# Kernel tuning notes

Measured on AMD Instinct MI355X. Metric: run time of the kernel, lower is better.

The kernel has to match this reference:

```python
import jax, jax.numpy as jnp
import numpy as np

B, D_IN, D_OUT, E = 8192, 1024, 1024, 16

def setup_inputs() -> dict:
    key = jax.random.key(0)
    k1, k2, k3 = jax.random.split(key, 3)
    scale_in = 1.0 / np.sqrt(D_IN)
    return {
        "x": jax.random.normal(k1, (B, D_IN), dtype=jnp.float32),
        "Wg": jax.random.normal(k2, (D_IN, E), dtype=jnp.float32) * scale_in,
        "bg": jnp.zeros((E,), dtype=jnp.float32),
        "We": jax.random.normal(k3, (E, D_IN, D_OUT), dtype=jnp.float32) * scale_in,
        "be": jnp.zeros((E, D_OUT), dtype=jnp.float32),
    }

def reference(x, Wg, bg, We, be):
    # gate: Linear + softmax over experts  -> [B, E]
    gate_probs = jax.nn.softmax(x @ Wg + bg, axis=1)
    # all experts as one batched GEMM: [B, E, D_OUT]
    expert_outputs = jnp.einsum("bi,eio->beo", x, We) + be[None, :, :]
    # gate-weighted sum over experts -> [B, D_OUT]
    return jnp.einsum("be,beo->bo", gate_probs, expert_outputs)
```

## Files before the change

### kernel.cpp

```cpp
#include <hip/hip_runtime.h>
#include <hip/hip_bf16.h>

#define NB 8192
#define DIN 1024
#define DOUT 1024
#define NE 16

#define BM 256
#define BN 256
#define BK 64
#define NT 128

typedef __attribute__((ext_vector_type(8))) short bf16x8;
typedef __attribute__((ext_vector_type(4))) short short4_t;
typedef __attribute__((ext_vector_type(4))) float f32x4;

__device__ __forceinline__ unsigned short f32_to_bf16(float f) {
  unsigned int u = __float_as_uint(f);
  u += 0x7FFFu + ((u >> 16) & 1u);
  return (unsigned short)(u >> 16);
}

__device__ __forceinline__ void gl_lds16(const void* gp, void* lp) {
  __builtin_amdgcn_global_load_lds(
      (const __attribute__((address_space(1))) void*)gp,
      (__attribute__((address_space(3))) void*)lp, 16, 0, 0);
}

#define SB __builtin_amdgcn_sched_barrier(0)

__global__ __launch_bounds__(256) void gate_cast_kernel(
    const float* __restrict__ x, const float* __restrict__ Wg,
    const float* __restrict__ bg, float* __restrict__ gout,
    unsigned short* __restrict__ xbf) {
  const int lane = threadIdx.x & 63;
  const int wid = threadIdx.x >> 6;
  const int row = blockIdx.x * 4 + wid;

  const f32x4* xr = (const f32x4*)(x + (size_t)row * DIN);
  f32x4 xv[4];
#pragma unroll
  for (int j = 0; j < 4; ++j) xv[j] = xr[j * 64 + lane];

  float acc[NE];
#pragma unroll
  for (int e = 0; e < NE; ++e) acc[e] = 0.f;

#pragma unroll
  for (int j = 0; j < 4; ++j) {
#pragma unroll
    for (int t = 0; t < 4; ++t) {
      const int i = j * 256 + lane * 4 + t;
      const f32x4* wrow = (const f32x4*)(Wg + (size_t)i * NE);
      const f32x4 w0 = wrow[0], w1 = wrow[1], w2 = wrow[2], w3 = wrow[3];
      const float xx = xv[j][t];
#pragma unroll
      for (int q = 0; q < 4; ++q) {
        acc[q]      = fmaf(xx, w0[q], acc[q]);
        acc[4 + q]  = fmaf(xx, w1[q], acc[4 + q]);
        acc[8 + q]  = fmaf(xx, w2[q], acc[8 + q]);
        acc[12 + q] = fmaf(xx, w3[q], acc[12 + q]);
      }
    }
  }
#pragma unroll
  for (int off = 32; off >= 1; off >>= 1) {
#pragma unroll
    for (int e = 0; e < NE; ++e) acc[e] += __shfl_xor(acc[e], off, 64);
  }
#pragma unroll
  for (int e = 0; e < NE; ++e) acc[e] += bg[e];
  float mx = acc[0];
#pragma unroll
  for (int e = 1; e < NE; ++e) mx = fmaxf(mx, acc[e]);
  float p[NE];
  float s = 0.f;
#pragma unroll
  for (int e = 0; e < NE; ++e) { p[e] = expf(acc[e] - mx); s += p[e]; }
  const float inv = 1.f / s;
  if (lane == 0) {
#pragma unroll
    for (int e = 0; e < NE; ++e) gout[(size_t)row * NE + e] = p[e] * inv;
  }
#pragma unroll
  for (int j = 0; j < 4; ++j) {
    short4_t o;
#pragma unroll
    for (int t = 0; t < 4; ++t) o[t] = (short)f32_to_bf16(xv[j][t]);
    *(short4_t*)(xbf + (size_t)row * DIN + j * 256 + lane * 4) = o;
  }
}

__global__ __launch_bounds__(256) void we_transpose_kernel(
    const float* __restrict__ We, unsigned short* __restrict__ WeT) {
  __shared__ float tile[64][65];
  const int e = blockIdx.z, it = blockIdx.y, ot = blockIdx.x;
  const int tr = threadIdx.x >> 4;
  const int tc = (threadIdx.x & 15) * 4;
  const float* src = We + (((size_t)e * DIN + it * 64) * DOUT) + ot * 64;
#pragma unroll
  for (int rr = 0; rr < 64; rr += 16) {
    const f32x4 v = *(const f32x4*)(src + (size_t)(rr + tr) * DOUT + tc);
#pragma unroll
    for (int t = 0; t < 4; ++t) tile[rr + tr][tc + t] = v[t];
  }
  __syncthreads();
  unsigned short* dst = WeT + (((size_t)e * DOUT + ot * 64) * DIN) + it * 64;
#pragma unroll
  for (int rr = 0; rr < 64; rr += 16) {
    short4_t o;
#pragma unroll
    for (int t = 0; t < 4; ++t) o[t] = (short)f32_to_bf16(tile[tc + t][rr + tr]);
    *(short4_t*)(dst + (size_t)(rr + tr) * DIN + tc) = o;
  }
}

__global__ __launch_bounds__(512, 2) void moe_gemm_kernel(
    const unsigned short* __restrict__ xbf,
    const unsigned short* __restrict__ WeT,
    const float* __restrict__ g,
    const float* __restrict__ be,
    float* __restrict__ out0,
    float* __restrict__ out1) {
  __shared__ __align__(16) unsigned short As[2][BM * BK];
  __shared__ __align__(16) unsigned short Bs[2][BN * BK];
  __shared__ float gs[BM][NE];

  const int tid = threadIdx.x;
  const int lane = tid & 63, wid = tid >> 6;
  const int wm = wid >> 2, wn = wid & 3;
  const int l15 = lane & 15, l4 = lane >> 4;

  const int bid = blockIdx.x;
  const int xcd = bid & 7, jj_ = bid >> 3;
  const int kh = xcd >> 2;
  const int brow = ((xcd & 3) * 8 + (jj_ >> 2)) * BM;
  const int bcol = (jj_ & 3) * BN;
  float* const outp = kh ? out1 : out0;

  const int swz0 = (l4 * 16) ^ ((l15 & 7) << 4);
  const int swz1 = (64 + l4 * 16) ^ ((l15 & 7) << 4);
  const char* const ldsA0 = (const char*)&As[0][0] + (wm * 128 + l15) * 128 + swz0;
  const char* const ldsA1 = (const char*)&As[0][0] + (wm * 128 + l15) * 128 + swz1;
  const char* const ldsB0 = (const char*)&Bs[0][0] + (wn * 64 + l15) * 128 + swz0;
  const char* const ldsB1 = (const char*)&Bs[0][0] + (wn * 64 + l15) * 128 + swz1;

  const int srow = tid >> 3;
  const int lk = (((tid & 7) * 16) ^ ((srow & 7) << 4)) >> 1;
  const unsigned short* const aBase = xbf + (size_t)(brow + srow) * DIN + lk;
  const unsigned short* const bBase = WeT + (size_t)(bcol + srow) * DIN + lk;
  char* const ldsStA = (char*)&As[0][0] + wid * 1024;
  char* const ldsStB = (char*)&Bs[0][0] + wid * 1024;

#define STA(BUF, CR, KC) \
  gl_lds16(aBase + (size_t)(CR) * DIN + (KC), ldsStA + (BUF) * 32768 + (CR) * 128)
#define STB(BUF, CR, EOFF, KC) \
  gl_lds16(bBase + (EOFF) + (size_t)(CR) * DIN + (KC), \
           ldsStB + (BUF) * 32768 + (CR) * 128)
#define RD_B(KS, BUF)                                             \
  _Pragma("unroll") for (int ni = 0; ni < 4; ++ni)                \
      bfr[ni][KS] = *(const bf16x8*)(((KS) ? ldsB1 : ldsB0) +     \
                                     ni * 2048 + (BUF) * 32768);
#define RD_A(KS, MI0, BUF)                                        \
  _Pragma("unroll") for (int d = 0; d < 4; ++d)                   \
      af[d] = *(const bf16x8*)(((KS) ? ldsA1 : ldsA0) +           \
                               ((MI0) + d) * 2048 + (BUF) * 32768);
#define MFMA_P(MI0, KS)                                            \
  _Pragma("unroll") for (int d = 0; d < 4; ++d)                    \
  _Pragma("unroll") for (int ni = 0; ni < 4; ++ni)                 \
      acc[(MI0) + d][ni] = __builtin_amdgcn_mfma_f32_16x16x32_bf16(\
          af[d], bfr[ni][KS], acc[(MI0) + d][ni], 0, 0, 0);

  {
    const f32x4* gsrc = (const f32x4*)(g + (size_t)brow * NE);
    f32x4* gdst = (f32x4*)&gs[0][0];
    gdst[tid] = gsrc[tid];
    gdst[tid + 512] = gsrc[tid + 512];
  }

  {
    const size_t e0 = (size_t)(kh * 8) * (size_t)(DIN * DOUT);
    STB(0, 0, e0, 0);  STB(0, 128, e0, 0);
    STB(0, 64, e0, 0); STB(0, 192, e0, 0);
    STA(0, 0, 0);      STA(0, 128, 0);
    STA(0, 64, 0);     STA(0, 192, 0);
  }

  f32x4 acc[8][4];
#pragma unroll
  for (int mi = 0; mi < 8; ++mi)
#pragma unroll
    for (int ni = 0; ni < 4; ++ni) acc[mi][ni] = (f32x4){0.f, 0.f, 0.f, 0.f};

  asm volatile("s_waitcnt vmcnt(2) lgkmcnt(0)" ::: "memory");
  SB; __builtin_amdgcn_s_barrier(); SB;

  bf16x8 bfr[4][2], af[4];

#define TILE_BODY(T, BUF)                                                      \
  {                                                                            \
    const int t_ = (T);                                                        \
    const int kcN = ((t_ + 1) & 15) * 64;                                      \
    const size_t eoffN =                                                       \
        (size_t)(kh * 8 + ((t_ + 1) >> 4)) * (size_t)(DIN * DOUT);             \
    const bool hasNext = (t_ + 1) < NT;                                        \
    if ((t_ & 15) == 0 && t_ > 0) {               \
      const int e = kh * 8 + (t_ >> 4);                                        \
      _Pragma("unroll") for (int mi = 0; mi < 8; ++mi) {                       \
        const int rb = wm * 128 + mi * 16 + l4 * 4;                            \
        _Pragma("unroll") for (int q = 0; q < 4; ++q) {                        \
          const float r = gs[rb + q][e - 1] *                                  \
                          __builtin_amdgcn_rcpf(fmaxf(gs[rb + q][e], 1e-30f)); \
          _Pragma("unroll") for (int ni = 0; ni < 4; ++ni)                     \
              acc[mi][ni][q] *= r;                                             \
        }                                                                      \
      }                                                                        \
    }                                                                          \
                                               \
    RD_B(0, BUF); RD_A(0, 0, BUF);                                             \
    if (hasNext) { STB(BUF ^ 1, 0, eoffN, kcN); STB(BUF ^ 1, 128, eoffN, kcN); } \
    SB; __builtin_amdgcn_s_barrier(); SB;                                      \
    __builtin_amdgcn_s_setprio(1); MFMA_P(0, 0);                               \
    __builtin_amdgcn_s_setprio(0); SB;                                         \
                                               \
    RD_B(1, BUF); RD_A(1, 0, BUF);                                             \
    if (hasNext) { STB(BUF ^ 1, 64, eoffN, kcN); STB(BUF ^ 1, 192, eoffN, kcN); } \
    if (t_ == NT - 1) { asm volatile("s_waitcnt vmcnt(0)" ::: "memory"); }     \
    else { asm volatile("s_waitcnt vmcnt(4)" ::: "memory"); }                  \
    SB; __builtin_amdgcn_s_barrier(); SB;                                      \
    __builtin_amdgcn_s_setprio(1); MFMA_P(0, 1);                               \
    __builtin_amdgcn_s_setprio(0); SB;                                         \
                                               \
    RD_A(0, 4, BUF);                                                           \
    if (hasNext) { STA(BUF ^ 1, 0, kcN); STA(BUF ^ 1, 128, kcN); }             \
    SB; __builtin_amdgcn_s_barrier(); SB;                                      \
    __builtin_amdgcn_s_setprio(1); MFMA_P(4, 0);                               \
    __builtin_amdgcn_s_setprio(0); SB;                                         \
                                               \
    RD_A(1, 4, BUF);                                                           \
    if (hasNext) { STA(BUF ^ 1, 64, kcN); STA(BUF ^ 1, 192, kcN); }            \
    SB; __builtin_amdgcn_s_barrier(); SB;                                      \
    __builtin_amdgcn_s_setprio(1); MFMA_P(4, 1);                               \
    __builtin_amdgcn_s_setprio(0);                                             \
    if ((t_ & 15) == 15) {                              \
      const int e = kh * 8 + (t_ >> 4);                                        \
      _Pragma("unroll") for (int ni = 0; ni < 4; ++ni) {                       \
        const float bv = be[e * DOUT + bcol + wn * 64 + ni * 16 + l15];        \
        _Pragma("unroll") for (int mi = 0; mi < 8; ++mi)                       \
          _Pragma("unroll") for (int q = 0; q < 4; ++q)                        \
              acc[mi][ni][q] += bv;                                            \
      }                                                                        \
    }                                                                          \
    if (t_ < NT - 1) { asm volatile("s_waitcnt vmcnt(2)" ::: "memory"); }      \
    SB; __builtin_amdgcn_s_barrier(); SB;                                      \
  }

  for (int tt = 0; tt < NT; tt += 2) {
    TILE_BODY(tt, 0);
    TILE_BODY(tt + 1, 1);
  }

  const int eL = kh * 8 + 7;
#pragma unroll
  for (int mi = 0; mi < 8; ++mi) {
    const int rb = wm * 128 + mi * 16 + l4 * 4;
#pragma unroll
    for (int q = 0; q < 4; ++q) {
      const float gf = gs[rb + q][eL];
      const size_t orow = (size_t)brow + rb + q;
#pragma unroll
      for (int ni = 0; ni < 4; ++ni)
        outp[orow * DOUT + bcol + wn * 64 + ni * 16 + l15] =
            acc[mi][ni][q] * gf;
    }
  }
#undef TILE_BODY
#undef MFMA_P
#undef RD_A
#undef RD_B
#undef STA
#undef STB
}

__global__ __launch_bounds__(256) void combine_kernel(
    float* __restrict__ out, const float* __restrict__ p1) {
  const size_t i = (size_t)blockIdx.x * 256 + threadIdx.x;
  f32x4 a = ((const f32x4*)out)[i];
  const f32x4 b = ((const f32x4*)p1)[i];
#pragma unroll
  for (int q = 0; q < 4; ++q) a[q] += b[q];
  ((f32x4*)out)[i] = a;
}

extern "C" void kernel_launch(void* const* d_in, const int* in_sizes, int n_in,
                              void* d_out, int out_size, void* d_ws, size_t ws_size,
                              hipStream_t stream) {
  const float* x  = (const float*)d_in[0];
  const float* Wg = (const float*)d_in[1];
  const float* bg = (const float*)d_in[2];
  const float* We = (const float*)d_in[3];
  const float* be = (const float*)d_in[4];
  float* out = (float*)d_out;

  char* ws = (char*)d_ws;
  unsigned short* xbf = (unsigned short*)ws;
  unsigned short* WeT = (unsigned short*)(ws + (size_t)NB * DIN * 2);
  float* g = (float*)(ws + (size_t)NB * DIN * 2 + (size_t)NE * DIN * DOUT * 2);
  float* p1 = (float*)(ws + (size_t)NB * DIN * 2 + (size_t)NE * DIN * DOUT * 2 +
                       (size_t)NB * NE * 4);

  gate_cast_kernel<<<dim3(NB / 4), 256, 0, stream>>>(x, Wg, bg, g, xbf);
  we_transpose_kernel<<<dim3(DOUT / 64, DIN / 64, NE), 256, 0, stream>>>(We, WeT);
  moe_gemm_kernel<<<dim3(256), 512, 0, stream>>>(xbf, WeT, g, be, out, p1);
  combine_kernel<<<dim3(NB * DOUT / 4 / 256), 256, 0, stream>>>(out, p1);
}
```

Baseline: 340.0 us.

## Pre-pack expert weights in MFMA fragment order and load B directly to registers

```diff
diff --git a/kernel.cpp b/kernel.cpp
--- a/kernel.cpp
+++ b/kernel.cpp
@@ -25,6 +25,10 @@
   __builtin_amdgcn_global_load_lds(
       (const __attribute__((address_space(1))) void*)gp,
       (__attribute__((address_space(3))) void*)lp, 16, 0, 0);
+}
+
+__device__ __forceinline__ void gload16(bf16x8& d, const unsigned short* p) {
+  asm volatile("global_load_dwordx4 %0, %1, off" : "=v"(d) : "v"(p));
 }
 
 #define SB __builtin_amdgcn_sched_barrier(0)
@@ -91,13 +95,13 @@
   }
 }
 
-__global__ __launch_bounds__(256) void we_transpose_kernel(
-    const float* __restrict__ We, unsigned short* __restrict__ WeT) {
+__global__ __launch_bounds__(256) void we_pack_kernel(
+    const float* __restrict__ We, unsigned short* __restrict__ WeP) {
   __shared__ float tile[64][65];
-  const int e = blockIdx.z, it = blockIdx.y, ot = blockIdx.x;
+  const int e = blockIdx.z, kt = blockIdx.y, ot = blockIdx.x;
   const int tr = threadIdx.x >> 4;
   const int tc = (threadIdx.x & 15) * 4;
-  const float* src = We + (((size_t)e * DIN + it * 64) * DOUT) + ot * 64;
+  const float* src = We + (((size_t)e * DIN + kt * 64) * DOUT) + ot * 64;
 #pragma unroll
   for (int rr = 0; rr < 64; rr += 16) {
     const f32x4 v = *(const f32x4*)(src + (size_t)(rr + tr) * DOUT + tc);
@@ -105,25 +109,31 @@
     for (int t = 0; t < 4; ++t) tile[rr + tr][tc + t] = v[t];
   }
   __syncthreads();
-  unsigned short* dst = WeT + (((size_t)e * DOUT + ot * 64) * DIN) + it * 64;
-#pragma unroll
-  for (int rr = 0; rr < 64; rr += 16) {
-    short4_t o;
-#pragma unroll
-    for (int t = 0; t < 4; ++t) o[t] = (short)f32_to_bf16(tile[tc + t][rr + tr]);
-    *(short4_t*)(dst + (size_t)(rr + tr) * DIN + tc) = o;
+  unsigned short* const dst =
+      WeP + ((size_t)(e * 16 + kt) * 64 + ot * 4) * 1024;
+#pragma unroll
+  for (int h = 0; h < 2; ++h) {
+    const int c = (int)threadIdx.x + h * 256;
+    const int l = c & 63;
+    const int ks = (c >> 6) & 1;
+    const int cf = c >> 7;
+    const int o = cf * 16 + (l & 15);
+    const int i0 = ks * 32 + (l >> 4) * 8;
+    bf16x8 w;
+#pragma unroll
+    for (int j = 0; j < 8; ++j) w[j] = (short)f32_to_bf16(tile[i0 + j][o]);
+    *(bf16x8*)(dst + (size_t)c * 8) = w;
   }
 }
 
 __global__ __launch_bounds__(512, 2) void moe_gemm_kernel(
     const unsigned short* __restrict__ xbf,
-    const unsigned short* __restrict__ WeT,
+    const unsigned short* __restrict__ WeP,
     const float* __restrict__ g,
     const float* __restrict__ be,
     float* __restrict__ out0,
     float* __restrict__ out1) {
   __shared__ __align__(16) unsigned short As[2][BM * BK];
-  __shared__ __align__(16) unsigned short Bs[2][BN * BK];
   __shared__ float gs[BM][NE];
 
   const int tid = threadIdx.x;
@@ -140,36 +150,37 @@
 
   const int swz0 = (l4 * 16) ^ ((l15 & 7) << 4);
   const int swz1 = (64 + l4 * 16) ^ ((l15 & 7) << 4);
-  const char* const ldsA0 = (const char*)&As[0][0] + (wm * 128 + l15) * 128 + swz0;
-  const char* const ldsA1 = (const char*)&As[0][0] + (wm * 128 + l15) * 128 + swz1;
-  const char* const ldsB0 = (const char*)&Bs[0][0] + (wn * 64 + l15) * 128 + swz0;
-  const char* const ldsB1 = (const char*)&Bs[0][0] + (wn * 64 + l15) * 128 + swz1;
+  const char* const ldsA0 =
+      (const char*)&As[0][0] + (wm * 128 + l15) * 128 + swz0;
+  const char* const ldsA1 =
+      (const char*)&As[0][0] + (wm * 128 + l15) * 128 + swz1;
 
   const int srow = tid >> 3;
   const int lk = (((tid & 7) * 16) ^ ((srow & 7) << 4)) >> 1;
   const unsigned short* const aBase = xbf + (size_t)(brow + srow) * DIN + lk;
-  const unsigned short* const bBase = WeT + (size_t)(bcol + srow) * DIN + lk;
   char* const ldsStA = (char*)&As[0][0] + wid * 1024;
-  char* const ldsStB = (char*)&Bs[0][0] + wid * 1024;
+
+  const unsigned short* const bBase0 = WeP + (size_t)kh * 128 * 65536 +
+                                       (size_t)(bcol / 16 + wn * 4) * 1024 +
+                                       (size_t)lane * 8;
 
 #define STA(BUF, CR, KC) \
-  gl_lds16(aBase + (size_t)(CR) * DIN + (KC), ldsStA + (BUF) * 32768 + (CR) * 128)
-#define STB(BUF, CR, EOFF, KC) \
-  gl_lds16(bBase + (EOFF) + (size_t)(CR) * DIN + (KC), \
-           ldsStB + (BUF) * 32768 + (CR) * 128)
-#define RD_B(KS, BUF)                                             \
-  _Pragma("unroll") for (int ni = 0; ni < 4; ++ni)                \
-      bfr[ni][KS] = *(const bf16x8*)(((KS) ? ldsB1 : ldsB0) +     \
-                                     ni * 2048 + (BUF) * 32768);
-#define RD_A(KS, MI0, BUF)                                        \
-  _Pragma("unroll") for (int d = 0; d < 4; ++d)                   \
-      af[d] = *(const bf16x8*)(((KS) ? ldsA1 : ldsA0) +           \
+  gl_lds16(aBase + (size_t)(CR) * DIN + (KC), \
+           ldsStA + (BUF) * 32768 + (CR) * 128)
+#define RD_A(KS, MI0, BUF)                                  \
+  _Pragma("unroll") for (int d = 0; d < 4; ++d)             \
+      af[d] = *(const bf16x8*)(((KS) ? ldsA1 : ldsA0) +     \
                                ((MI0) + d) * 2048 + (BUF) * 32768);
-#define MFMA_P(MI0, KS)                                            \
+#define LOADB8(NXT, BP)                                           \
+  gload16(NXT[0][0], (BP)); gload16(NXT[0][1], (BP) + 512);       \
+  gload16(NXT[1][0], (BP) + 1024); gload16(NXT[1][1], (BP) + 1536); \
+  gload16(NXT[2][0], (BP) + 2048); gload16(NXT[2][1], (BP) + 2560); \
+  gload16(NXT[3][0], (BP) + 3072); gload16(NXT[3][1], (BP) + 3584);
+#define MFMA_P(MI0, KS, BF)                                        \
   _Pragma("unroll") for (int d = 0; d < 4; ++d)                    \
   _Pragma("unroll") for (int ni = 0; ni < 4; ++ni)                 \
       acc[(MI0) + d][ni] = __builtin_amdgcn_mfma_f32_16x16x32_bf16(\
-          af[d], bfr[ni][KS], acc[(MI0) + d][ni], 0, 0, 0);
+          af[d], BF[ni][KS], acc[(MI0) + d][ni], 0, 0, 0);
 
   {
     const f32x4* gsrc = (const f32x4*)(g + (size_t)brow * NE);
@@ -178,13 +189,11 @@
     gdst[tid + 512] = gsrc[tid + 512];
   }
 
-  {
-    const size_t e0 = (size_t)(kh * 8) * (size_t)(DIN * DOUT);
-    STB(0, 0, e0, 0);  STB(0, 128, e0, 0);
-    STB(0, 64, e0, 0); STB(0, 192, e0, 0);
-    STA(0, 0, 0);      STA(0, 128, 0);
-    STA(0, 64, 0);     STA(0, 192, 0);
-  }
+  bf16x8 bA[4][2], bB[4][2], af[4];
+
+  LOADB8(bA, bBase0);
+  STA(0, 0, 0); STA(0, 128, 0);
+  STA(0, 64, 0); STA(0, 192, 0);
 
   f32x4 acc[8][4];
 #pragma unroll
@@ -195,14 +204,9 @@
   asm volatile("s_waitcnt vmcnt(2) lgkmcnt(0)" ::: "memory");
   SB; __builtin_amdgcn_s_barrier(); SB;
 
-  bf16x8 bfr[4][2], af[4];
-
-#define TILE_BODY(T, BUF)                                                      \
+#define TILE_BODY(T, BUF, CUR, NXT)                                            \
   {                                                                            \
     const int t_ = (T);                                                        \
-    const int kcN = ((t_ + 1) & 15) * 64;                                      \
-    const size_t eoffN =                                                       \
-        (size_t)(kh * 8 + ((t_ + 1) >> 4)) * (size_t)(DIN * DOUT);             \
     const bool hasNext = (t_ + 1) < NT;                                        \
     if ((t_ & 15) == 0 && t_ > 0) {               \
       const int e = kh * 8 + (t_ >> 4);                                        \
@@ -216,70 +220,79 @@
         }                                                                      \
       }                                                                        \
     }                                                                          \
-                                               \
-    RD_B(0, BUF); RD_A(0, 0, BUF);                                             \
-    if (hasNext) { STB(BUF ^ 1, 0, eoffN, kcN); STB(BUF ^ 1, 128, eoffN, kcN); } \
+                          \
+    if (hasNext) {                                                             \
+      const unsigned short* bp = bBase0 + (size_t)(t_ + 1) * 65536;            \
+      LOADB8(NXT, bp);                                                         \
+    }                                                                          \
+    RD_A(0, 0, BUF);                                                           \
+    __builtin_amdgcn_s_setprio(1); MFMA_P(0, 0, CUR);                          \
+    __builtin_amdgcn_s_setprio(0);                                             \
+    RD_A(1, 0, BUF);                                                           \
+    __builtin_amdgcn_s_setprio(1); MFMA_P(0, 1, CUR);                          \
+    __builtin_amdgcn_s_setprio(0);                                             \
+    if (hasNext) { asm volatile("s_waitcnt vmcnt(8)" ::: "memory"); }          \
+    else         { asm volatile("s_waitcnt vmcnt(0)" ::: "memory"); }          \
     SB; __builtin_amdgcn_s_barrier(); SB;                                      \
-    __builtin_amdgcn_s_setprio(1); MFMA_P(0, 0);                               \
-    __builtin_amdgcn_s_setprio(0); SB;                                         \
-                                               \
-    RD_B(1, BUF); RD_A(1, 0, BUF);                                             \
-    if (hasNext) { STB(BUF ^ 1, 64, eoffN, kcN); STB(BUF ^ 1, 192, eoffN, kcN); } \
-    if (t_ == NT - 1) { asm volatile("s_waitcnt vmcnt(0)" ::: "memory"); }     \
-    else { asm volatile("s_waitcnt vmcnt(4)" ::: "memory"); }                  \
-    SB; __builtin_amdgcn_s_barrier(); SB;                                      \
-    __builtin_amdgcn_s_setprio(1); MFMA_P(0, 1);                               \
-    __builtin_amdgcn_s_setprio(0); SB;                                         \
-                                               \
+                             \
+    if (hasNext) {                                                             \
+      const int kcN = ((t_ + 1) & 15) * 64;                                    \
+      STA(BUF ^ 1, 0, kcN); STA(BUF ^ 1, 128, kcN);                            \
+      STA(BUF ^ 1, 64, kcN); STA(BUF ^ 1, 192, kcN);                           \
+    }                                                                          \
     RD_A(0, 4, BUF);                                                           \
-    if (hasNext) { STA(BUF ^ 1, 0, kcN); STA(BUF ^ 1, 128, kcN); }             \
-    SB; __builtin_amdgcn_s_barrier(); SB;                                      \
-    __builtin_amdgcn_s_setprio(1); MFMA_P(4, 0);                               \
-    __builtin_amdgcn_s_setprio(0); SB;                                         \
-                                               \
+    __builtin_amdgcn_s_setprio(1); MFMA_P(4, 0, CUR);                          \
+    __builtin_amdgcn_s_setprio(0);                                             \
     RD_A(1, 4, BUF);                                                           \
-    if (hasNext) { STA(BUF ^ 1, 64, kcN); STA(BUF ^ 1, 192, kcN); }            \
-    SB; __builtin_amdgcn_s_barrier(); SB;                                      \
-    __builtin_amdgcn_s_setprio(1); MFMA_P(4, 1);                               \
+    __builtin_amdgcn_s_setprio(1); MFMA_P(4, 1, CUR);                          \
     __builtin_amdgcn_s_setprio(0);                                             \
-    if ((t_ & 15) == 15) {                              \
-      const int e = kh * 8 + (t_ >> 4);                                        \
-      _Pragma("unroll") for (int ni = 0; ni < 4; ++ni) {                       \
-        const float bv = be[e * DOUT + bcol + wn * 64 + ni * 16 + l15];        \
-        _Pragma("unroll") for (int mi = 0; mi < 8; ++mi)                       \
-          _Pragma("unroll") for (int q = 0; q < 4; ++q)                        \
-              acc[mi][ni][q] += bv;                                            \
-      }                                                                        \
+    if (hasNext) {                                                             \
+      asm volatile("s_waitcnt vmcnt(2)" ::: "memory");                         \
+      SB; __builtin_amdgcn_s_barrier(); SB;                                    \
     }                                                                          \
-    if (t_ < NT - 1) { asm volatile("s_waitcnt vmcnt(2)" ::: "memory"); }      \
-    SB; __builtin_amdgcn_s_barrier(); SB;                                      \
   }
 
   for (int tt = 0; tt < NT; tt += 2) {
-    TILE_BODY(tt, 0);
-    TILE_BODY(tt + 1, 1);
+    TILE_BODY(tt, 0, bA, bB);
+    TILE_BODY(tt + 1, 1, bB, bA);
   }
 
   const int eL = kh * 8 + 7;
+  float bv[8][4];
+#pragma unroll
+  for (int e8 = 0; e8 < 8; ++e8)
+#pragma unroll
+    for (int ni = 0; ni < 4; ++ni)
+      bv[e8][ni] = be[(kh * 8 + e8) * DOUT + bcol + wn * 64 + ni * 16 + l15];
 #pragma unroll
   for (int mi = 0; mi < 8; ++mi) {
     const int rb = wm * 128 + mi * 16 + l4 * 4;
 #pragma unroll
     for (int q = 0; q < 4; ++q) {
-      const float gf = gs[rb + q][eL];
-      const size_t orow = (size_t)brow + rb + q;
-#pragma unroll
-      for (int ni = 0; ni < 4; ++ni)
-        outp[orow * DOUT + bcol + wn * 64 + ni * 16 + l15] =
-            acc[mi][ni][q] * gf;
+      const int row = rb + q;
+      const float gf = gs[row][eL];
+      float b0 = 0.f, b1 = 0.f, b2 = 0.f, b3 = 0.f;
+#pragma unroll
+      for (int e8 = 0; e8 < 8; ++e8) {
+        const float ge = gs[row][kh * 8 + e8];
+        b0 = fmaf(ge, bv[e8][0], b0);
+        b1 = fmaf(ge, bv[e8][1], b1);
+        b2 = fmaf(ge, bv[e8][2], b2);
+        b3 = fmaf(ge, bv[e8][3], b3);
+      }
+      const size_t orow = (size_t)brow + row;
+      float* const orp = outp + orow * DOUT + bcol + wn * 64 + l15;
+      orp[0]  = fmaf(acc[mi][0][q], gf, b0);
+      orp[16] = fmaf(acc[mi][1][q], gf, b1);
+      orp[32] = fmaf(acc[mi][2][q], gf, b2);
+      orp[48] = fmaf(acc[mi][3][q], gf, b3);
     }
   }
 #undef TILE_BODY
 #undef MFMA_P
+#undef LOADB8
 #undef RD_A
-#undef RD_B
 #undef STA
-#undef STB
 }
 
 __global__ __launch_bounds__(256) void combine_kernel(
@@ -304,13 +317,13 @@
 
   char* ws = (char*)d_ws;
   unsigned short* xbf = (unsigned short*)ws;
-  unsigned short* WeT = (unsigned short*)(ws + (size_t)NB * DIN * 2);
+  unsigned short* WeP = (unsigned short*)(ws + (size_t)NB * DIN * 2);
   float* g = (float*)(ws + (size_t)NB * DIN * 2 + (size_t)NE * DIN * DOUT * 2);
   float* p1 = (float*)(ws + (size_t)NB * DIN * 2 + (size_t)NE * DIN * DOUT * 2 +
                        (size_t)NB * NE * 4);
 
   gate_cast_kernel<<<dim3(NB / 4), 256, 0, stream>>>(x, Wg, bg, g, xbf);
-  we_transpose_kernel<<<dim3(DOUT / 64, DIN / 64, NE), 256, 0, stream>>>(We, WeT);
-  moe_gemm_kernel<<<dim3(256), 512, 0, stream>>>(xbf, WeT, g, be, out, p1);
+  we_pack_kernel<<<dim3(DOUT / 64, DIN / 64, NE), 256, 0, stream>>>(We, WeP);
+  moe_gemm_kernel<<<dim3(256), 512, 0, stream>>>(xbf, WeP, g, be, out, p1);
   combine_kernel<<<dim3(NB * DOUT / 4 / 256), 256, 0, stream>>>(out, p1);
 }
```

New measurement: 347.1 us. 1.02x slower.

## Switch MoE GEMM to 32x32x16 MFMA with fewer barriers and epilogue bias

Applied to the files above, without the earlier changes.

```diff
diff --git a/kernel.cpp b/kernel.cpp
--- a/kernel.cpp
+++ b/kernel.cpp
@@ -14,6 +14,7 @@
 typedef __attribute__((ext_vector_type(8))) short bf16x8;
 typedef __attribute__((ext_vector_type(4))) short short4_t;
 typedef __attribute__((ext_vector_type(4))) float f32x4;
+typedef __attribute__((ext_vector_type(16))) float f32x16;
 
 __device__ __forceinline__ unsigned short f32_to_bf16(float f) {
   unsigned int u = __float_as_uint(f);
@@ -129,7 +130,7 @@
   const int tid = threadIdx.x;
   const int lane = tid & 63, wid = tid >> 6;
   const int wm = wid >> 2, wn = wid & 3;
-  const int l15 = lane & 15, l4 = lane >> 4;
+  const int l31 = lane & 31, lh = lane >> 5;
 
   const int bid = blockIdx.x;
   const int xcd = bid & 7, jj_ = bid >> 3;
@@ -138,12 +139,12 @@
   const int bcol = (jj_ & 3) * BN;
   float* const outp = kh ? out1 : out0;
 
-  const int swz0 = (l4 * 16) ^ ((l15 & 7) << 4);
-  const int swz1 = (64 + l4 * 16) ^ ((l15 & 7) << 4);
-  const char* const ldsA0 = (const char*)&As[0][0] + (wm * 128 + l15) * 128 + swz0;
-  const char* const ldsA1 = (const char*)&As[0][0] + (wm * 128 + l15) * 128 + swz1;
-  const char* const ldsB0 = (const char*)&Bs[0][0] + (wn * 64 + l15) * 128 + swz0;
-  const char* const ldsB1 = (const char*)&Bs[0][0] + (wn * 64 + l15) * 128 + swz1;
+  const int swz = (l31 & 7) << 4;
+  int offK[4];
+#pragma unroll
+  for (int ks = 0; ks < 4; ++ks) offK[ks] = ((ks << 5) | (lh << 4)) ^ swz;
+  const char* const ldsA = (const char*)&As[0][0] + (wm * 128 + l31) * 128;
+  const char* const ldsB = (const char*)&Bs[0][0] + (wn * 64 + l31) * 128;
 
   const int srow = tid >> 3;
   const int lk = (((tid & 7) * 16) ^ ((srow & 7) << 4)) >> 1;
@@ -153,23 +154,25 @@
   char* const ldsStB = (char*)&Bs[0][0] + wid * 1024;
 
 #define STA(BUF, CR, KC) \
-  gl_lds16(aBase + (size_t)(CR) * DIN + (KC), ldsStA + (BUF) * 32768 + (CR) * 128)
+  gl_lds16(aBase + (size_t)(CR) * DIN + (KC), \
+           ldsStA + (BUF) * 32768 + (CR) * 128)
 #define STB(BUF, CR, EOFF, KC) \
   gl_lds16(bBase + (EOFF) + (size_t)(CR) * DIN + (KC), \
            ldsStB + (BUF) * 32768 + (CR) * 128)
-#define RD_B(KS, BUF)                                             \
-  _Pragma("unroll") for (int ni = 0; ni < 4; ++ni)                \
-      bfr[ni][KS] = *(const bf16x8*)(((KS) ? ldsB1 : ldsB0) +     \
-                                     ni * 2048 + (BUF) * 32768);
-#define RD_A(KS, MI0, BUF)                                        \
-  _Pragma("unroll") for (int d = 0; d < 4; ++d)                   \
-      af[d] = *(const bf16x8*)(((KS) ? ldsA1 : ldsA0) +           \
-                               ((MI0) + d) * 2048 + (BUF) * 32768);
-#define MFMA_P(MI0, KS)                                            \
-  _Pragma("unroll") for (int d = 0; d < 4; ++d)                    \
-  _Pragma("unroll") for (int ni = 0; ni < 4; ++ni)                 \
-      acc[(MI0) + d][ni] = __builtin_amdgcn_mfma_f32_16x16x32_bf16(\
-          af[d], bfr[ni][KS], acc[(MI0) + d][ni], 0, 0, 0);
+#define RD_B(BUF)                                                   \
+  _Pragma("unroll") for (int ni = 0; ni < 2; ++ni)                  \
+  _Pragma("unroll") for (int ks = 0; ks < 4; ++ks)                  \
+      bfr[ni][ks] = *(const bf16x8*)(ldsB + (BUF) * 32768 +         \
+                                     ni * 4096 + offK[ks]);
+#define RD_A(MI, SLOT, BUF)                                         \
+  _Pragma("unroll") for (int ks = 0; ks < 4; ++ks)                  \
+      afr[SLOT][ks] = *(const bf16x8*)(ldsA + (BUF) * 32768 +       \
+                                       (MI) * 4096 + offK[ks]);
+#define MFMA8(MI, SLOT)                                             \
+  _Pragma("unroll") for (int ks = 0; ks < 4; ++ks)                  \
+  _Pragma("unroll") for (int ni = 0; ni < 2; ++ni)                  \
+      acc[MI][ni] = __builtin_amdgcn_mfma_f32_32x32x16_bf16(        \
+          afr[SLOT][ks], bfr[ni][ks], acc[MI][ni], 0, 0, 0);
 
   {
     const f32x4* gsrc = (const f32x4*)(g + (size_t)brow * NE);
@@ -180,79 +183,64 @@
 
   {
     const size_t e0 = (size_t)(kh * 8) * (size_t)(DIN * DOUT);
-    STB(0, 0, e0, 0);  STB(0, 128, e0, 0);
-    STB(0, 64, e0, 0); STB(0, 192, e0, 0);
-    STA(0, 0, 0);      STA(0, 128, 0);
-    STA(0, 64, 0);     STA(0, 192, 0);
-  }
-
-  f32x4 acc[8][4];
-#pragma unroll
-  for (int mi = 0; mi < 8; ++mi)
-#pragma unroll
-    for (int ni = 0; ni < 4; ++ni) acc[mi][ni] = (f32x4){0.f, 0.f, 0.f, 0.f};
+    STB(0, 0, e0, 0); STB(0, 64, e0, 0);
+    STB(0, 128, e0, 0); STB(0, 192, e0, 0);
+    STA(0, 0, 0); STA(0, 128, 0);
+    STA(0, 64, 0); STA(0, 192, 0);
+  }
+
+  f32x16 acc[4][2];
+#pragma unroll
+  for (int mi = 0; mi < 4; ++mi)
+#pragma unroll
+    for (int ni = 0; ni < 2; ++ni)
+#pragma unroll
+      for (int r = 0; r < 16; ++r) acc[mi][ni][r] = 0.f;
 
   asm volatile("s_waitcnt vmcnt(2) lgkmcnt(0)" ::: "memory");
   SB; __builtin_amdgcn_s_barrier(); SB;
 
-  bf16x8 bfr[4][2], af[4];
+  bf16x8 bfr[2][4], afr[2][4];
 
 #define TILE_BODY(T, BUF)                                                      \
   {                                                                            \
     const int t_ = (T);                                                        \
+    const bool hasNext = (t_ + 1) < NT;                                        \
     const int kcN = ((t_ + 1) & 15) * 64;                                      \
     const size_t eoffN =                                                       \
         (size_t)(kh * 8 + ((t_ + 1) >> 4)) * (size_t)(DIN * DOUT);             \
-    const bool hasNext = (t_ + 1) < NT;                                        \
     if ((t_ & 15) == 0 && t_ > 0) {               \
       const int e = kh * 8 + (t_ >> 4);                                        \
-      _Pragma("unroll") for (int mi = 0; mi < 8; ++mi) {                       \
-        const int rb = wm * 128 + mi * 16 + l4 * 4;                            \
-        _Pragma("unroll") for (int q = 0; q < 4; ++q) {                        \
-          const float r = gs[rb + q][e - 1] *                                  \
-                          __builtin_amdgcn_rcpf(fmaxf(gs[rb + q][e], 1e-30f)); \
-          _Pragma("unroll") for (int ni = 0; ni < 4; ++ni)                     \
-              acc[mi][ni][q] *= r;                                             \
-        }                                                                      \
+      _Pragma("unroll") for (int mi = 0; mi < 4; ++mi)                         \
+      _Pragma("unroll") for (int r = 0; r < 16; ++r) {                         \
+        const int row = wm * 128 + mi * 32 + (r & 3) + 8 * (r >> 2) + 4 * lh;  \
+        const float ratio = gs[row][e - 1] *                                   \
+            __builtin_amdgcn_rcpf(fmaxf(gs[row][e], 1e-30f));                  \
+        acc[mi][0][r] *= ratio; acc[mi][1][r] *= ratio;                        \
       }                                                                        \
     }                                                                          \
-                                               \
-    RD_B(0, BUF); RD_A(0, 0, BUF);                                             \
-    if (hasNext) { STB(BUF ^ 1, 0, eoffN, kcN); STB(BUF ^ 1, 128, eoffN, kcN); } \
-    SB; __builtin_amdgcn_s_barrier(); SB;                                      \
-    __builtin_amdgcn_s_setprio(1); MFMA_P(0, 0);                               \
-    __builtin_amdgcn_s_setprio(0); SB;                                         \
-                                               \
-    RD_B(1, BUF); RD_A(1, 0, BUF);                                             \
-    if (hasNext) { STB(BUF ^ 1, 64, eoffN, kcN); STB(BUF ^ 1, 192, eoffN, kcN); } \
-    if (t_ == NT - 1) { asm volatile("s_waitcnt vmcnt(0)" ::: "memory"); }     \
-    else { asm volatile("s_waitcnt vmcnt(4)" ::: "memory"); }                  \
-    SB; __builtin_amdgcn_s_barrier(); SB;                                      \
-    __builtin_amdgcn_s_setprio(1); MFMA_P(0, 1);                               \
-    __builtin_amdgcn_s_setprio(0); SB;                                         \
-                                               \
-    RD_A(0, 4, BUF);                                                           \
-    if (hasNext) { STA(BUF ^ 1, 0, kcN); STA(BUF ^ 1, 128, kcN); }             \
-    SB; __builtin_amdgcn_s_barrier(); SB;                                      \
-    __builtin_amdgcn_s_setprio(1); MFMA_P(4, 0);                               \
-    __builtin_amdgcn_s_setprio(0); SB;                                         \
-                                               \
-    RD_A(1, 4, BUF);                                                           \
+                                       \
+    if (hasNext) {                                                             \
+      STB(BUF ^ 1, 0, eoffN, kcN); STB(BUF ^ 1, 64, eoffN, kcN);               \
+      STB(BUF ^ 1, 128, eoffN, kcN); STB(BUF ^ 1, 192, eoffN, kcN);            \
+      STA(BUF ^ 1, 0, kcN); STA(BUF ^ 1, 128, kcN);                            \
+    }                                                                          \
+                                            \
+    RD_B(BUF); RD_A(0, 0, BUF); RD_A(1, 1, BUF);                               \
+    __builtin_amdgcn_s_setprio(1); MFMA8(0, 0); MFMA8(1, 1);                   \
+    __builtin_amdgcn_s_setprio(0);                                             \
+    if (hasNext) { asm volatile("s_waitcnt vmcnt(6)" ::: "memory"); }          \
+    else         { asm volatile("s_waitcnt vmcnt(0)" ::: "memory"); }          \
+    SB;                                                                        \
     if (hasNext) { STA(BUF ^ 1, 64, kcN); STA(BUF ^ 1, 192, kcN); }            \
-    SB; __builtin_amdgcn_s_barrier(); SB;                                      \
-    __builtin_amdgcn_s_setprio(1); MFMA_P(4, 1);                               \
+                                                       \
+    RD_A(2, 0, BUF); RD_A(3, 1, BUF);                                          \
+    __builtin_amdgcn_s_setprio(1); MFMA8(2, 0); MFMA8(3, 1);                   \
     __builtin_amdgcn_s_setprio(0);                                             \
-    if ((t_ & 15) == 15) {                              \
-      const int e = kh * 8 + (t_ >> 4);                                        \
-      _Pragma("unroll") for (int ni = 0; ni < 4; ++ni) {                       \
-        const float bv = be[e * DOUT + bcol + wn * 64 + ni * 16 + l15];        \
-        _Pragma("unroll") for (int mi = 0; mi < 8; ++mi)                       \
-          _Pragma("unroll") for (int q = 0; q < 4; ++q)                        \
-              acc[mi][ni][q] += bv;                                            \
-      }                                                                        \
+    if (hasNext) {                                                             \
+      asm volatile("s_waitcnt vmcnt(2)" ::: "memory");                         \
+      SB; __builtin_amdgcn_s_barrier(); SB;                                    \
     }                                                                          \
-    if (t_ < NT - 1) { asm volatile("s_waitcnt vmcnt(2)" ::: "memory"); }      \
-    SB; __builtin_amdgcn_s_barrier(); SB;                                      \
   }
 
   for (int tt = 0; tt < NT; tt += 2) {
@@ -261,21 +249,32 @@
   }
 
   const int eL = kh * 8 + 7;
-#pragma unroll
-  for (int mi = 0; mi < 8; ++mi) {
-    const int rb = wm * 128 + mi * 16 + l4 * 4;
-#pragma unroll
-    for (int q = 0; q < 4; ++q) {
-      const float gf = gs[rb + q][eL];
-      const size_t orow = (size_t)brow + rb + q;
-#pragma unroll
-      for (int ni = 0; ni < 4; ++ni)
-        outp[orow * DOUT + bcol + wn * 64 + ni * 16 + l15] =
-            acc[mi][ni][q] * gf;
+  float bv[8][2];
+#pragma unroll
+  for (int e8 = 0; e8 < 8; ++e8)
+#pragma unroll
+    for (int ni = 0; ni < 2; ++ni)
+      bv[e8][ni] = be[(kh * 8 + e8) * DOUT + bcol + wn * 64 + ni * 32 + l31];
+#pragma unroll
+  for (int mi = 0; mi < 4; ++mi)
+#pragma unroll
+    for (int r = 0; r < 16; ++r) {
+      const int row = wm * 128 + mi * 32 + (r & 3) + 8 * (r >> 2) + 4 * lh;
+      const float gf = gs[row][eL];
+      float b0 = 0.f, b1 = 0.f;
+#pragma unroll
+      for (int e8 = 0; e8 < 8; ++e8) {
+        const float ge = gs[row][kh * 8 + e8];
+        b0 = fmaf(ge, bv[e8][0], b0);
+        b1 = fmaf(ge, bv[e8][1], b1);
+      }
+      float* const orp =
+          outp + (size_t)(brow + row) * DOUT + bcol + wn * 64 + l31;
+      orp[0]  = fmaf(acc[mi][0][r], gf, b0);
+      orp[32] = fmaf(acc[mi][1][r], gf, b1);
     }
-  }
 #undef TILE_BODY
-#undef MFMA_P
+#undef MFMA8
 #undef RD_A
 #undef RD_B
 #undef STA
```

After: 369.2 us. +8.6%, slower.
